# Kernel optimization log

Hardware: AMD Instinct MI355X
Metric: run time of the kernel (lower is better)

The kernel has to match this reference:

```python
import jax, jax.numpy as jnp
import numpy as np

B, T, E, V, L = 8, 128, 256, 8192, 5  # batch, block_size, embedding_size (== num heads, head_size=1), vocab, num blocks


def setup_inputs() -> dict:
    key = jax.random.key(0)
    ks = jax.random.split(key, 12)
    s = 0.02
    return {
        "idxs": jax.random.randint(ks[0], (B, T), 0, V),
        "targets": jax.random.randint(ks[1], (B, T), 0, V),
        "emb": jax.random.normal(ks[2], (V, E)) * s,
        "pos_emb": jax.random.normal(ks[3], (T, E)) * s,
        "Wq": jax.random.normal(ks[4], (L, E, E)) * s,  # per-layer: E heads, each Linear(E,1); columns are heads
        "Wk": jax.random.normal(ks[5], (L, E, E)) * s,
        "Wv": jax.random.normal(ks[6], (L, E, E)) * s,
        "Wfc": jax.random.normal(ks[7], (L, E, E)) * s,
        "bfc": jnp.zeros((L, E)),
        "Wlm": jax.random.normal(ks[8], (E, V)) * s,
        "blm": jnp.zeros((V,)),
    }


def _block(x, Wq, Wk, Wv, Wfc, bfc):
    # E heads of head_size=1: projecting with [E,E] gives [B,T,H] with H==E,
    # column h being head h's scalar q/k/v. Faithful to per-head Linear(E,1).
    q = x @ Wq
    k = x @ Wk
    v = x @ Wv
    scores = jnp.einsum('bih,bjh->bhij', q, k)  # no 1/sqrt(d) scaling (faithful)
    i = jnp.arange(x.shape[1])
    causal = i[:, None] >= i[None, :]  # masked_fill where tril==0, i.e. j>i -> -inf
    scores = jnp.where(causal[None, None], scores, -jnp.inf)
    attn = jax.nn.softmax(scores, axis=-2)  # NOTE: source softmaxes over dim=-2 (query axis) -- faithful quirk
    out = jnp.einsum('bhij,bjh->bih', attn, v)  # concat of heads == H axis order
    x = x + out
    return x + jax.nn.relu(x @ Wfc + bfc)


def reference(idxs, targets, emb, pos_emb, Wq, Wk, Wv, Wfc, bfc, Wlm, blm):
    x = emb[idxs] + pos_emb[: idxs.shape[1]]  # [B,T,E]
    for l in range(L):
        x = _block(x, Wq[l], Wk[l], Wv[l], Wfc[l], bfc[l])
    logits = (x @ Wlm + blm).reshape(-1, V)  # [B*T, V], as source views before CE
    logp = jax.nn.log_softmax(logits, axis=-1)
    loss = -jnp.take_along_axis(logp, targets.reshape(-1, 1), axis=-1).mean()
    return logits, loss
```

## Files before the change

### kernel.cpp

```cpp
#include <hip/hip_runtime.h>

#define BB 8
#define TT 128
#define EE 256
#define VV 8192
#define LL 5
#define NROWS (BB*TT)

typedef __attribute__((ext_vector_type(8))) short bf16x8;
typedef __attribute__((ext_vector_type(4))) float f32x4;

__device__ inline ushort f2bf(float f) {
    union { float f; unsigned u; } c; c.f = f;
    unsigned u = c.u;
    return (ushort)((u + 0x7FFF + ((u >> 16) & 1)) >> 16);
}

__global__ __launch_bounds__(256) void prep_kernel(
        const int* __restrict__ idxs, const float* __restrict__ emb, const float* __restrict__ pos,
        const float* __restrict__ Wq, const float* __restrict__ Wk,
        const float* __restrict__ Wv, const float* __restrict__ Wfc,
        const float* __restrict__ Wlm,
        float* __restrict__ x0, ushort* __restrict__ WTs, ushort* __restrict__ WlmT,
        float* __restrict__ loss_cell) {
    int id = blockIdx.x;
    if (id == 0) {
        if (threadIdx.x == 0) *loss_cell = 0.f;
        return;
    }
    if (id < 513) {
        __shared__ ushort ts[64][72];
        int idw = id - 1;
        int v0 = (idw & 127) * 64, k0 = (idw >> 7) * 64;
        int lane = threadIdx.x & 63, w = threadIdx.x >> 6;
        for (int kk = w; kk < 64; kk += 4)
            ts[lane][kk] = f2bf(Wlm[(size_t)(k0 + kk)*VV + v0 + lane]);
        __syncthreads();
        for (int vv = w; vv < 64; vv += 4)
            WlmT[(size_t)(v0 + vv)*EE + k0 + lane] = ts[vv][lane];
        return;
    }
    if (id < 833) {
        __shared__ ushort ts[64][72];
        int idm = id - 513;
        int mat = idm >> 4, tile = idm & 15;
        int l = mat >> 2, type = mat & 3;
        const float* src = (type == 0 ? Wq : type == 1 ? Wk : type == 2 ? Wv : Wfc) + l*EE*EE;
        ushort* dst = WTs + mat*EE*EE;
        int i0 = (tile >> 2) * 64, o0 = (tile & 3) * 64;
        int lane = threadIdx.x & 63, w = threadIdx.x >> 6;
        for (int ii = w; ii < 64; ii += 4)
            ts[lane][ii] = f2bf(src[(i0 + ii)*EE + o0 + lane]);
        __syncthreads();
        for (int oo = w; oo < 64; oo += 4)
            dst[(o0 + oo)*EE + i0 + lane] = ts[oo][lane];
        return;
    }
    int h = threadIdx.x;
    int row0 = (id - 833) * 4;
    for (int r = 0; r < 4; ++r) {
        int row = row0 + r;
        x0[row*EE + h] = emb[(size_t)idxs[row]*EE + h] + pos[(row & (TT-1))*EE + h];
    }
}

__global__ __launch_bounds__(512, 4) void qkv_attn_kernel(
        float* __restrict__ x, const ushort* __restrict__ WTl) {
    __shared__ __align__(16) ushort Xs[128*128];
    __shared__ __align__(16) ushort Bs[32*128];
    __shared__ float QS[8*132], KS[8*132], VS[8*132], MS[8*132], RV[8*132];
    int tid = threadIdx.x, lane = tid & 63, w = tid >> 6;
    int b  = blockIdx.x >> 5;
    int h0 = (blockIdx.x & 31) * 8;

    f32x4 acc[2] = {};
    int rband = w*16 + (lane & 15);
    int kq = (lane >> 4) * 8;

    #pragma unroll
    for (int half = 0; half < 2; ++half) {
        if (half) __syncthreads();
        {
            int rsub = lane >> 5, cb = (lane & 31) * 4;
            for (int rr2 = w*2; rr2 < 128; rr2 += 16) {
                int rr = rr2 + rsub;
                float4 v = *(const float4*)&x[(size_t)(b*TT + rr)*EE + half*128 + cb];
                ushort4 hh; hh.x = f2bf(v.x); hh.y = f2bf(v.y); hh.z = f2bf(v.z); hh.w = f2bf(v.w);
                *(ushort4*)&Xs[rr*128 + (cb ^ ((rr & 7) << 3))] = hh;
            }
        }
        {
            int c = tid >> 4;
            int kb = (tid & 15) * 8;
            uint4 v0 = make_uint4(0,0,0,0);
            if (c < 24) {
                int mat = c >> 3;
                int col = h0 + (c & 7);
                v0 = *(const uint4*)&WTl[(size_t)mat*EE*EE + (size_t)col*EE + half*128 + kb];
            }
            *(uint4*)&Bs[c*128 + (kb ^ ((c & 7) << 3))] = v0;
        }
        __syncthreads();
        for (int ks = 0; ks < 4; ++ks) {
            int kk = ks*32 + kq;
            bf16x8 a = *(const bf16x8*)&Xs[rband*128 + (kk ^ ((rband & 7) << 3))];
            #pragma unroll
            for (int ct = 0; ct < 2; ++ct) {
                int c = ct*16 + (lane & 15);
                bf16x8 bb = *(const bf16x8*)&Bs[c*128 + (kk ^ ((c & 7) << 3))];
                acc[ct] = __builtin_amdgcn_mfma_f32_16x16x32_bf16(a, bb, acc[ct], 0, 0, 0);
            }
        }
    }
    {
        int r_ = w*16 + ((lane >> 4) << 2);
        #pragma unroll
        for (int ct = 0; ct < 2; ++ct) {
            int col24 = ct*16 + (lane & 15);
            #pragma unroll
            for (int j = 0; j < 4; ++j) {
                float val = acc[ct][j];
                int row = r_ + j;
                if (col24 < 8)       QS[col24*132 + row] = val;
                else if (col24 < 16) KS[(col24-8)*132 + row] = val;
                else if (col24 < 24) VS[(col24-16)*132 + row] = val;
            }
        }
    }
    __syncthreads();

    int g = w, lg = lane;
    {
        int j0 = lg*2;
        float k0 = KS[g*132 + j0], k1 = KS[g*132 + j0 + 1];
        float q0j = QS[g*132 + j0], q1j = QS[g*132 + j0 + 1];
        float pmax = fmaxf(q0j, q1j), pmin = fminf(q0j, q1j);
        #pragma unroll
        for (int d = 1; d < 64; d <<= 1) {
            float om = __shfl_down(pmax, d);
            float on = __shfl_down(pmin, d);
            if (lg + d < 64) { pmax = fmaxf(pmax, om); pmin = fminf(pmin, on); }
        }
        float nx = __shfl_down(pmax, 1), nn = __shfl_down(pmin, 1);
        float sp1 = (lg == 63) ? q1j : fmaxf(q1j, nx);
        float sn1 = (lg == 63) ? q1j : fminf(q1j, nn);
        float m0 = (k0 >= 0.f) ? k0*pmax : k0*pmin;
        float m1 = (k1 >= 0.f) ? k1*sp1  : k1*sn1;
        float z0 = 0.f, z1 = 0.f;
        for (int i = j0; i < TT; ++i) {
            float qi = QS[g*132 + i];
            z0 += __expf(qi*k0 - m0);
            z1 += (i >= j0+1) ? __expf(qi*k1 - m1) : 0.f;
        }
        MS[g*132 + j0]     = m0;
        MS[g*132 + j0 + 1] = m1;
        RV[g*132 + j0]     = VS[g*132 + j0] / z0;
        RV[g*132 + j0 + 1] = VS[g*132 + j0 + 1] / z1;
    }
    __syncthreads();
    float a0 = 0.f, a1 = 0.f;
    {
        int i0 = lg*2;
        float q0 = QS[g*132 + i0], q1 = QS[g*132 + i0 + 1];
        for (int j = 0; j <= i0 + 1; ++j) {
            float kj = KS[g*132 + j], mj = MS[g*132 + j], rj = RV[g*132 + j];
            float e0 = __expf(q0*kj - mj) * rj;
            float e1 = __expf(q1*kj - mj) * rj;
            a0 += (j <= i0) ? e0 : 0.f;
            a1 += e1;
        }
    }
    __syncthreads();
    VS[g*132 + lg*2]     = a0;
    VS[g*132 + lg*2 + 1] = a1;
    __syncthreads();

    {
        int row = tid >> 2, cp = (tid & 3) * 2;
        size_t gx = (size_t)(b*TT + row)*EE + h0 + cp;
        float2 xv = *(float2*)&x[gx];
        xv.x += VS[cp*132 + row];
        xv.y += VS[(cp+1)*132 + row];
        *(float2*)&x[gx] = xv;
    }
}

__global__ __launch_bounds__(256) void fc_mfma(
        const float* __restrict__ xin, const ushort* __restrict__ WT,
        const float* __restrict__ bfc, float* __restrict__ xout) {
    __shared__ __align__(16) ushort As[64*256];
    __shared__ __align__(16) ushort Bs[64*256];
    int tid = threadIdx.x, lane = tid & 63, w = tid >> 6;
    int c0 = blockIdx.x * 64;
    int r0 = blockIdx.y * 64;

    for (int rr = w; rr < 64; rr += 4) {
        float4 v = *(const float4*)&xin[(size_t)(r0 + rr)*EE + lane*4];
        ushort4 hh; hh.x = f2bf(v.x); hh.y = f2bf(v.y); hh.z = f2bf(v.z); hh.w = f2bf(v.w);
        *(ushort4*)&As[rr*256 + ((lane*4) ^ ((rr & 7) << 3))] = hh;
    }
    for (int it = 0; it < 8; ++it) {
        int c = w*16 + (lane >> 5) + 2*it;
        int k0i = (lane & 31) * 8;
        uint4 v = *(const uint4*)&WT[(size_t)(c0 + c)*EE + k0i];
        *(uint4*)&Bs[c*256 + (k0i ^ ((c & 7) << 3))] = v;
    }
    __syncthreads();
    f32x4 acc[4] = {};
    int rband = w*16 + (lane & 15);
    int kq = (lane >> 4) * 8;
    for (int ks = 0; ks < 8; ++ks) {
        int kk = ks*32 + kq;
        bf16x8 a = *(const bf16x8*)&As[rband*256 + (kk ^ ((rband & 7) << 3))];
        #pragma unroll
        for (int n = 0; n < 4; ++n) {
            int c = n*16 + (lane & 15);
            bf16x8 b = *(const bf16x8*)&Bs[c*256 + (kk ^ ((c & 7) << 3))];
            acc[n] = __builtin_amdgcn_mfma_f32_16x16x32_bf16(a, b, acc[n], 0, 0, 0);
        }
    }
    int grow0 = r0 + w*16 + ((lane >> 4) << 2);
    #pragma unroll
    for (int n = 0; n < 4; ++n) {
        int col = c0 + n*16 + (lane & 15);
        float bias = bfc[col];
        #pragma unroll
        for (int j = 0; j < 4; ++j) {
            size_t idx = (size_t)(grow0 + j)*EE + col;
            xout[idx] = xin[idx] + fmaxf(acc[n][j] + bias, 0.f);
        }
    }
}

__global__ __launch_bounds__(512, 4) void lm_mfma_kernel(
        const float* __restrict__ x, const ushort* __restrict__ WlmT,
        const float* __restrict__ blm, float* __restrict__ out,
        float* __restrict__ pm, float* __restrict__ pz) {
    __shared__ __align__(16) char LDSb[128*132*4];
    ushort* As = (ushort*)LDSb;
    ushort* Bs = (ushort*)LDSb + 128*128;
    float*  fst = (float*)LDSb;
    int tid = threadIdx.x;
    int lane = tid & 63, w = tid >> 6;
    int c0 = blockIdx.x * 128;
    int r0 = blockIdx.y * 128;

    int wr = (w >> 2) * 64, wc = (w & 3) * 32;
    f32x4 acc[4][2] = {};
    int kq = (lane >> 4) * 8;

    #pragma unroll
    for (int half = 0; half < 2; ++half) {
        if (half) __syncthreads();
        {
            int rsub = lane >> 5, cb = (lane & 31) * 4;
            for (int rr2 = w*2; rr2 < 128; rr2 += 16) {
                int rr = rr2 + rsub;
                float4 v = *(const float4*)&x[(size_t)(r0 + rr)*EE + half*128 + cb];
                ushort4 hh; hh.x = f2bf(v.x); hh.y = f2bf(v.y); hh.z = f2bf(v.z); hh.w = f2bf(v.w);
                *(ushort4*)&As[rr*128 + (cb ^ ((rr & 7) << 3))] = hh;
            }
        }
        {
            int csub = lane >> 5, kb = (lane & 31) * 4;
        }
        {
            int c = tid >> 4;
            int kb = (tid & 15) * 8;
            #pragma unroll
            for (int cg = 0; cg < 4; ++cg) {
                int cc = cg*32 + c;
                uint4 v = *(const uint4*)&WlmT[(size_t)(c0 + cc)*EE + half*128 + kb];
                *(uint4*)&Bs[cc*128 + (kb ^ ((cc & 7) << 3))] = v;
            }
        }
        __syncthreads();
        for (int ks = 0; ks < 4; ++ks) {
            int kk = ks*32 + kq;
            bf16x8 a[4], bfr[2];
            #pragma unroll
            for (int m = 0; m < 4; ++m) {
                int rband = wr + m*16 + (lane & 15);
                a[m] = *(const bf16x8*)&As[rband*128 + (kk ^ ((rband & 7) << 3))];
            }
            #pragma unroll
            for (int n = 0; n < 2; ++n) {
                int c = wc + n*16 + (lane & 15);
                bfr[n] = *(const bf16x8*)&Bs[c*128 + (kk ^ ((c & 7) << 3))];
            }
            #pragma unroll
            for (int m = 0; m < 4; ++m)
                #pragma unroll
                for (int n = 0; n < 2; ++n)
                    acc[m][n] = __builtin_amdgcn_mfma_f32_16x16x32_bf16(a[m], bfr[n], acc[m][n], 0, 0, 0);
        }
    }
    __syncthreads();

    float bias[2];
    #pragma unroll
    for (int n = 0; n < 2; ++n) bias[n] = blm[c0 + wc + n*16 + (lane & 15)];
    #pragma unroll
    for (int m = 0; m < 4; ++m) {
        int rw = wr + m*16 + (lane >> 4)*4;
        #pragma unroll
        for (int j = 0; j < 4; ++j) {
            int row = rw + j;
            float vals[2];
            float vmax = -INFINITY;
            #pragma unroll
            for (int n = 0; n < 2; ++n) {
                vals[n] = acc[m][n][j] + bias[n];
                fst[row*132 + wc + n*16 + (lane & 15)] = vals[n];
                vmax = fmaxf(vmax, vals[n]);
            }
            #pragma unroll
            for (int msk = 1; msk <= 8; msk <<= 1) vmax = fmaxf(vmax, __shfl_xor(vmax, msk));
            float z = 0.f;
            #pragma unroll
            for (int n = 0; n < 2; ++n) z += __expf(vals[n] - vmax);
            #pragma unroll
            for (int msk = 1; msk <= 8; msk <<= 1) z += __shfl_xor(z, msk);
            if ((lane & 15) == 0) {
                pm[(size_t)(r0 + row)*256 + blockIdx.x*4 + (w & 3)] = vmax;
                pz[(size_t)(r0 + row)*256 + blockIdx.x*4 + (w & 3)] = z;
            }
        }
    }
    __syncthreads();
    #pragma unroll
    for (int it = 0; it < 8; ++it) {
        int k = tid + it*512;
        int row = k >> 5, c4 = (k & 31)*4;
        float4 v = *(float4*)&fst[row*132 + c4];
        *(float4*)&out[(size_t)(r0 + row)*VV + c0 + c4] = v;
    }
}

__global__ void loss_kernel(const float* __restrict__ pm, const float* __restrict__ pz,
                            const float* __restrict__ logits, const int* __restrict__ targets,
                            float* __restrict__ out_last) {
    int r = blockIdx.x;
    int t = threadIdx.x;
    __shared__ float sm[256], sz[256];
    float m = pm[(size_t)r*256 + t];
    float z = pz[(size_t)r*256 + t];
    sm[t] = m; __syncthreads();
    for (int s = 128; s > 0; s >>= 1) {
        if (t < s) sm[t] = fmaxf(sm[t], sm[t + s]);
        __syncthreads();
    }
    float M = sm[0];
    sz[t] = z * __expf(m - M); __syncthreads();
    for (int s = 128; s > 0; s >>= 1) {
        if (t < s) sz[t] += sz[t + s];
        __syncthreads();
    }
    if (t == 0) {
        float lse = M + logf(sz[0]);
        atomicAdd(out_last, (lse - logits[(size_t)r*VV + targets[r]]) * (1.0f / NROWS));
    }
}

extern "C" void kernel_launch(void* const* d_in, const int* in_sizes, int n_in,
                              void* d_out, int out_size, void* d_ws, size_t ws_size,
                              hipStream_t stream) {
    const int*   idxs    = (const int*)d_in[0];
    const int*   targets = (const int*)d_in[1];
    const float* emb     = (const float*)d_in[2];
    const float* pos     = (const float*)d_in[3];
    const float* Wq      = (const float*)d_in[4];
    const float* Wk      = (const float*)d_in[5];
    const float* Wv      = (const float*)d_in[6];
    const float* Wfc     = (const float*)d_in[7];
    const float* bfc     = (const float*)d_in[8];
    const float* Wlm     = (const float*)d_in[9];
    const float* blm     = (const float*)d_in[10];
    float* out = (float*)d_out;
    float* loss_cell = out + (size_t)NROWS * VV;

    float* ws = (float*)d_ws;
    float*  xa   = ws;
    float*  xb   = xa + NROWS*EE;
    float*  pm   = xb + NROWS*EE;
    float*  pz   = pm + NROWS*256;
    ushort* WTs  = (ushort*)(pz + NROWS*256);
    ushort* WlmT = WTs + 20*EE*EE;

    prep_kernel<<<1089, 256, 0, stream>>>(idxs, emb, pos, Wq, Wk, Wv, Wfc, Wlm,
                                          xa, WTs, WlmT, loss_cell);

    for (int l = 0; l < LL; ++l) {
        float* xi = (l & 1) ? xb : xa;
        float* xo = (l & 1) ? xa : xb;
        qkv_attn_kernel<<<256, 512, 0, stream>>>(xi, WTs + (size_t)l*4*EE*EE);
        fc_mfma<<<dim3(4, 16), 256, 0, stream>>>(xi, WTs + (size_t)(l*4 + 3)*EE*EE,
                                                 bfc + l*EE, xo);
    }

    lm_mfma_kernel<<<dim3(VV/128, NROWS/128), 512, 0, stream>>>(xb, WlmT, blm, out, pm, pz);
    loss_kernel<<<NROWS, 256, 0, stream>>>(pm, pz, out, targets, loss_cell);
}
```

Before: 203.4 us.

## Pre-swizzle transposed weights and load them directly into LDS

New measurement: 204.2 us. About the same (+0.4%).

```diff
diff --git a/kernel.cpp b/kernel.cpp
--- a/kernel.cpp
+++ b/kernel.cpp
@@ -15,6 +15,13 @@
     unsigned u = c.u;
     return (ushort)((u + 0x7FFF + ((u >> 16) & 1)) >> 16);
 }
+
+__device__ __forceinline__ void gload_lds16(const void* g, void* l) {
+    __builtin_amdgcn_global_load_lds((const __attribute__((address_space(1))) unsigned int*)g,
+                                     (__attribute__((address_space(3))) unsigned int*)l,
+                                     16, 0, 0);
+}
+
 
 __global__ __launch_bounds__(256) void prep_kernel(
         const int* __restrict__ idxs, const float* __restrict__ emb, const float* __restrict__ pos,
@@ -36,8 +43,10 @@
         for (int kk = w; kk < 64; kk += 4)
             ts[lane][kk] = f2bf(Wlm[(size_t)(k0 + kk)*VV + v0 + lane]);
         __syncthreads();
-        for (int vv = w; vv < 64; vv += 4)
-            WlmT[(size_t)(v0 + vv)*EE + k0 + lane] = ts[vv][lane];
+        for (int vv = w; vv < 64; vv += 4) {
+            int r = v0 + vv, k = k0 + lane;
+            WlmT[(size_t)r*256 + (k & 128) + ((k & 127) ^ ((r & 7) << 3))] = ts[vv][lane];
+        }
         return;
     }
     if (id < 833) {
@@ -52,8 +61,10 @@
         for (int ii = w; ii < 64; ii += 4)
             ts[lane][ii] = f2bf(src[(i0 + ii)*EE + o0 + lane]);
         __syncthreads();
-        for (int oo = w; oo < 64; oo += 4)
-            dst[(o0 + oo)*EE + i0 + lane] = ts[oo][lane];
+        for (int oo = w; oo < 64; oo += 4) {
+            int r = o0 + oo, k = i0 + lane;
+            dst[(size_t)r*256 + (k & 128) + ((k & 127) ^ ((r & 7) << 3))] = ts[oo][lane];
+        }
         return;
     }
     int h = threadIdx.x;
@@ -90,15 +101,12 @@
             }
         }
         {
-            int c = tid >> 4;
-            int kb = (tid & 15) * 8;
-            uint4 v0 = make_uint4(0,0,0,0);
-            if (c < 24) {
-                int mat = c >> 3;
-                int col = h0 + (c & 7);
-                v0 = *(const uint4*)&WTl[(size_t)mat*EE*EE + (size_t)col*EE + half*128 + kb];
-            }
-            *(uint4*)&Bs[c*128 + (kb ^ ((c & 7) << 3))] = v0;
+            int rowg = w*4 + (lane >> 4);
+            int rowv = rowg < 24 ? rowg : 23;
+            int mat = rowv >> 3, col = h0 + (rowv & 7);
+            const ushort* src = WTl + (size_t)mat*EE*EE + (size_t)col*256
+                              + half*128 + (lane & 15)*8;
+            gload_lds16(src, &Bs[w*4*128]);
         }
         __syncthreads();
         for (int ks = 0; ks < 4; ++ks) {
@@ -185,38 +193,46 @@
     }
 }
 
-__global__ __launch_bounds__(256) void fc_mfma(
+__global__ __launch_bounds__(256, 4) void fc_mfma(
         const float* __restrict__ xin, const ushort* __restrict__ WT,
         const float* __restrict__ bfc, float* __restrict__ xout) {
-    __shared__ __align__(16) ushort As[64*256];
-    __shared__ __align__(16) ushort Bs[64*256];
+    __shared__ __align__(16) ushort As[64*128];
+    __shared__ __align__(16) ushort Bs[64*128];
     int tid = threadIdx.x, lane = tid & 63, w = tid >> 6;
     int c0 = blockIdx.x * 64;
     int r0 = blockIdx.y * 64;
 
-    for (int rr = w; rr < 64; rr += 4) {
-        float4 v = *(const float4*)&xin[(size_t)(r0 + rr)*EE + lane*4];
-        ushort4 hh; hh.x = f2bf(v.x); hh.y = f2bf(v.y); hh.z = f2bf(v.z); hh.w = f2bf(v.w);
-        *(ushort4*)&As[rr*256 + ((lane*4) ^ ((rr & 7) << 3))] = hh;
-    }
-    for (int it = 0; it < 8; ++it) {
-        int c = w*16 + (lane >> 5) + 2*it;
-        int k0i = (lane & 31) * 8;
-        uint4 v = *(const uint4*)&WT[(size_t)(c0 + c)*EE + k0i];
-        *(uint4*)&Bs[c*256 + (k0i ^ ((c & 7) << 3))] = v;
-    }
-    __syncthreads();
     f32x4 acc[4] = {};
     int rband = w*16 + (lane & 15);
     int kq = (lane >> 4) * 8;
-    for (int ks = 0; ks < 8; ++ks) {
-        int kk = ks*32 + kq;
-        bf16x8 a = *(const bf16x8*)&As[rband*256 + (kk ^ ((rband & 7) << 3))];
-        #pragma unroll
-        for (int n = 0; n < 4; ++n) {
-            int c = n*16 + (lane & 15);
-            bf16x8 b = *(const bf16x8*)&Bs[c*256 + (kk ^ ((c & 7) << 3))];
-            acc[n] = __builtin_amdgcn_mfma_f32_16x16x32_bf16(a, b, acc[n], 0, 0, 0);
+
+    #pragma unroll
+    for (int half = 0; half < 2; ++half) {
+        if (half) __syncthreads();
+        {
+            int rsub = lane >> 5, cb = (lane & 31) * 4;
+            for (int rr2 = w*2; rr2 < 64; rr2 += 8) {
+                int rr = rr2 + rsub;
+                float4 v = *(const float4*)&xin[(size_t)(r0 + rr)*EE + half*128 + cb];
+                ushort4 hh; hh.x = f2bf(v.x); hh.y = f2bf(v.y); hh.z = f2bf(v.z); hh.w = f2bf(v.w);
+                *(ushort4*)&As[rr*128 + (cb ^ ((rr & 7) << 3))] = hh;
+            }
+        }
+        for (int rg = w*4; rg < 64; rg += 16) {
+            int row = c0 + rg + (lane >> 4);
+            const ushort* src = WT + (size_t)row*256 + half*128 + (lane & 15)*8;
+            gload_lds16(src, &Bs[rg*128]);
+        }
+        __syncthreads();
+        for (int ks = 0; ks < 4; ++ks) {
+            int kk = ks*32 + kq;
+            bf16x8 a = *(const bf16x8*)&As[rband*128 + (kk ^ ((rband & 7) << 3))];
+            #pragma unroll
+            for (int n = 0; n < 4; ++n) {
+                int c = n*16 + (lane & 15);
+                bf16x8 b = *(const bf16x8*)&Bs[c*128 + (kk ^ ((c & 7) << 3))];
+                acc[n] = __builtin_amdgcn_mfma_f32_16x16x32_bf16(a, b, acc[n], 0, 0, 0);
+            }
         }
     }
     int grow0 = r0 + w*16 + ((lane >> 4) << 2);
@@ -261,18 +277,10 @@
                 *(ushort4*)&As[rr*128 + (cb ^ ((rr & 7) << 3))] = hh;
             }
         }
-        {
-            int csub = lane >> 5, kb = (lane & 31) * 4;
-        }
-        {
-            int c = tid >> 4;
-            int kb = (tid & 15) * 8;
-            #pragma unroll
-            for (int cg = 0; cg < 4; ++cg) {
-                int cc = cg*32 + c;
-                uint4 v = *(const uint4*)&WlmT[(size_t)(c0 + cc)*EE + half*128 + kb];
-                *(uint4*)&Bs[cc*128 + (kb ^ ((cc & 7) << 3))] = v;
-            }
+        for (int rg = w*4; rg < 128; rg += 32) {
+            int row = c0 + rg + (lane >> 4);
+            const ushort* src = WlmT + (size_t)row*256 + half*128 + (lane & 15)*8;
+            gload_lds16(src, &Bs[rg*128]);
         }
         __syncthreads();
         for (int ks = 0; ks < 4; ++ks) {
```
